# Kernel tuning notes

Measured on AMD Instinct MI355X. Metric: run time of the kernel, lower is better.

## Reference

```python
import jax, jax.numpy as jnp
import numpy as np

B, T, DM, DS = 8, 2048, 1024, 256
BASE_DECAY = 0.05


def _lin(k, out_dim, in_dim):
    return jax.random.normal(k, (out_dim, in_dim), jnp.float32) / np.sqrt(in_dim).astype(np.float32)


def setup_inputs() -> dict:
    key = jax.random.key(0)
    ks = jax.random.split(key, 18)
    return {
        "x": jax.random.normal(ks[0], (B, T, DM), jnp.float32),
        "prev_state": jax.random.normal(ks[1], (B, DS), jnp.float32),
        "W_in": _lin(ks[2], DS, DM),
        "W_x": _lin(ks[3], DS, DM),
        "W_s": _lin(ks[4], DS, DS),
        "W_out": _lin(ks[5], DM, DS),
        "W_gx": _lin(ks[6], DS, DM),
        "b_gx": jax.random.normal(ks[7], (DS,), jnp.float32) * 0.02,
        "W_gs": _lin(ks[8], DS, DS),
        "b_gs": jax.random.normal(ks[9], (DS,), jnp.float32) * 0.02,
        "W_dc": _lin(ks[10], DS, DM + DS),
        "b_dc": jax.random.normal(ks[11], (DS,), jnp.float32) * 0.02,
        "W_pp": _lin(ks[12], DS, 2 * DS),
        "b_pp": jax.random.normal(ks[13], (DS,), jnp.float32) * 0.02,
        "W_pg": _lin(ks[14], DS, DS),
        "b_pg": jax.random.normal(ks[15], (DS,), jnp.float32) * 0.02,
    }


def reference(x, prev_state, W_in, W_x, W_s, W_out, W_gx, b_gx, W_gs, b_gs,
              W_dc, b_dc, W_pp, b_pp, W_pg, b_pg):
    # torch Linear: y = x @ W.T (+ b); W is [out, in]
    lin = lambda v, W: jnp.einsum('bti,oi->bto', v, W)
    Bx, Tx, _ = x.shape
    delta = lin(x, W_in)                                   # [B,T,DS]
    s_prev = jnp.broadcast_to(prev_state[:, None, :], (Bx, Tx, prev_state.shape[-1]))
    ctx = jnp.concatenate([x, s_prev], axis=-1)            # [B,T,DM+DS]
    decay = jnp.exp(-BASE_DECAY * jnp.clip(jax.nn.sigmoid(lin(ctx, W_dc) + b_dc), 0.0, 1.0))
    s_pred = s_prev * decay + delta + lin(x, W_x) + 0.5 * lin(s_prev, W_s)
    perturb_in = jnp.concatenate([s_pred, s_prev], axis=-1)  # [B,T,2*DS]
    perturb_vec = jnp.tanh(lin(perturb_in, W_pp) + b_pp)
    perturb_strength = jax.nn.sigmoid(lin(s_prev, W_pg) + b_pg)
    s_corrected = s_pred + perturb_strength * perturb_vec
    gate_in = jax.nn.sigmoid(lin(x, W_gx) + b_gx)
    gate_state = jax.nn.sigmoid(lin(s_prev, W_gs) + b_gs)
    h = s_corrected * gate_in * gate_state
    out = lin(h, W_out)                                    # [B,T,DM]
    return out, h[:, -1, :]
```

## Files before the change

kernel.cpp:

```cpp
#include <hip/hip_runtime.h>
#include <hip/hip_bf16.h>
#include <math.h>


typedef __attribute__((ext_vector_type(4)))  float f32x4;
typedef __attribute__((ext_vector_type(8)))  short bf16x8;

#define DEV static __device__ __forceinline__

DEV float bf2f(short u) {
  union { float f; unsigned i; } v; v.i = ((unsigned)(unsigned short)u) << 16; return v.f;
}
DEV short f2bf(float f) {
  union { float f; unsigned i; } v; v.f = f;
  unsigned x = v.i;
  return (short)((x + 0x7fffu + ((x >> 16) & 1u)) >> 16);
}
DEV unsigned pk_bf16(float lo, float hi) {
  __hip_bfloat162 h = __float22bfloat162_rn(make_float2(lo, hi));
  return *(unsigned*)&h;
}
DEV float sigmoidf_(float x) { return 1.f / (1.f + expf(-x)); }

DEV void gl16(const short* g, short* l) {
  __builtin_amdgcn_global_load_lds(
      (const __attribute__((address_space(1))) void*)(g),
      (__attribute__((address_space(3))) void*)(l), 16, 0, 0);
}

DEV void stage_tile(const short* gA, const short* gB, short* As, short* Bs,
                    int lda, int ldb, int w, int lane) {
  const int rsub = lane >> 2, kc = (lane & 3) * 8;
#pragma unroll
  for (int j = 0; j < 2; ++j) {
    const int seg = w * 2 + j;
    const int r = seg * 16 + rsub;
    gl16(gA + (size_t)r * lda + kc, As + seg * 512);
    gl16(gB + (size_t)r * ldb + kc, Bs + seg * 512);
  }
}

DEV void kstep(const short* Asb, const short* Bsb, int wr, int wc, int arow, int ag,
               f32x4 (&acc)[4][4]) {
  bf16x8 af[4], bfv[4];
#pragma unroll
  for (int mi = 0; mi < 4; ++mi)
    af[mi] = *(const bf16x8*)(Asb + (wr * 64 + mi * 16 + arow) * 32 + ag * 8);
#pragma unroll
  for (int ni = 0; ni < 4; ++ni)
    bfv[ni] = *(const bf16x8*)(Bsb + (wc * 64 + ni * 16 + arow) * 32 + ag * 8);
#pragma unroll
  for (int mi = 0; mi < 4; ++mi)
#pragma unroll
    for (int ni = 0; ni < 4; ++ni)
      acc[mi][ni] = __builtin_amdgcn_mfma_f32_16x16x32_bf16(af[mi], bfv[ni], acc[mi][ni], 0, 0, 0);
}

static const size_t OFF_Y    = 0;
static const size_t OFF_S    = 25165824;
static const size_t OFF_G    = OFF_S + 8388608;
static const size_t OFF_WCAT = OFF_S + 33554432;
static const size_t OFF_WPP  = OFF_WCAT + 1572864;
static const size_t OFF_WOUT = OFF_WPP + 131072;
static const size_t OFF_VEC  = OFF_WOUT + 524288;

__global__ __launch_bounds__(256, 1) void prep_w_k(const float* __restrict__ W_in,
                                                   const float* __restrict__ W_x,
                                                   const float* __restrict__ W_gx,
                                                   const float* __restrict__ W_dc,
                                                   const float* __restrict__ W_pp,
                                                   const float* __restrict__ W_out,
                                                   short* __restrict__ wcat,
                                                   short* __restrict__ wpp,
                                                   short* __restrict__ wout) {
  const int idx = (int)blockIdx.x * 256 + (int)threadIdx.x;
  const int N_WCAT = 768 * 1024, N_WPP = 256 * 256;
  if (idx < N_WCAT) {
    const int r = idx >> 10, k = idx & 1023;
    float v;
    if (r < 256)      v = W_in[r * 1024 + k] + W_x[r * 1024 + k];
    else if (r < 512) v = W_gx[(r - 256) * 1024 + k];
    else              v = W_dc[(r - 512) * 1280 + k];
    wcat[idx] = f2bf(v);
  } else if (idx < N_WCAT + N_WPP) {
    const int j = idx - N_WCAT, o = j >> 8, k = j & 255;
    wpp[j] = f2bf(W_pp[o * 512 + k]);
  } else {
    const int j = idx - N_WCAT - N_WPP, o = j >> 8, k = j & 255;
    wout[j] = f2bf(W_out[o * 256 + k]);
  }
}

__global__ __launch_bounds__(256, 1) void state_k(const float* __restrict__ prev,
                                                  const float* __restrict__ Ws,
                                                  const float* __restrict__ Wdc,
                                                  const float* __restrict__ bdc,
                                                  const float* __restrict__ Wpp,
                                                  const float* __restrict__ bpp,
                                                  const float* __restrict__ Wpg,
                                                  const float* __restrict__ bpg,
                                                  const float* __restrict__ Wgs,
                                                  const float* __restrict__ bgs,
                                                  float* __restrict__ vecs) {
  const int bid = (int)blockIdx.x;
  const int b = bid / 20, rem = bid % 20, m = rem >> 2, oq = rem & 3;
  const int tid = (int)threadIdx.x, lane = tid & 63, w = tid >> 6;
  const float4 sv = *(const float4*)(prev + b * 256 + lane * 4);
  const float* Wb; const float* bias; int stride, off;
  if (m == 0)      { Wb = Wdc; stride = 1280; off = 1024; bias = bdc; }
  else if (m == 1) { Wb = Ws;  stride = 256;  off = 0;    bias = nullptr; }
  else if (m == 2) { Wb = Wpp; stride = 512;  off = 256;  bias = bpp; }
  else if (m == 3) { Wb = Wpg; stride = 256;  off = 0;    bias = bpg; }
  else             { Wb = Wgs; stride = 256;  off = 0;    bias = bgs; }
  const int o0 = oq * 64 + w * 16;
#pragma unroll 4
  for (int i = 0; i < 16; ++i) {
    const int o = o0 + i;
    const float4 wv = *(const float4*)(Wb + (size_t)o * stride + off + lane * 4);
    float p = wv.x * sv.x + wv.y * sv.y + wv.z * sv.z + wv.w * sv.w;
#pragma unroll
    for (int d = 32; d >= 1; d >>= 1) p += __shfl_xor(p, d, 64);
    if (lane == 0) {
      float r = (m == 1) ? 0.5f * p : p + bias[o];
      if (m >= 3) r = sigmoidf_(r);
      vecs[m * 2048 + b * 256 + o] = r;
    }
  }
}

__global__ __launch_bounds__(256) void gemm1_k(const float* __restrict__ X,
                                               const short* __restrict__ Bm,
                                               short* __restrict__ Y) {
  __shared__ short As[2][4096];
  __shared__ short Bs[2][4096];
  const int tid = (int)threadIdx.x, lane = tid & 63, w = tid >> 6;
  const int wr = w >> 1, wc = w & 1;
  int bid = (int)blockIdx.x;
  bid = (bid & 7) * 96 + (bid >> 3);
  const int m0 = (bid / 6) * 128, n0 = (bid % 6) * 128;
  const short* gB = Bm + (size_t)n0 * 1024;

  const int rsub = lane >> 2, kc = (lane & 3) * 8;
  const float* gX0 = X + (size_t)(m0 + w * 32 + rsub) * 1024 + kc;
  const float* gX1 = X + (size_t)(m0 + w * 32 + 16 + rsub) * 1024 + kc;
  short* lA0 = (short*)As;

  f32x4 acc[4][4];
#pragma unroll
  for (int mi = 0; mi < 4; ++mi)
#pragma unroll
    for (int ni = 0; ni < 4; ++ni)
#pragma unroll
      for (int r = 0; r < 4; ++r) acc[mi][ni][r] = 0.f;

  float4 ra[2][2];
  ra[0][0] = *(const float4*)(gX0);     ra[0][1] = *(const float4*)(gX0 + 4);
  ra[1][0] = *(const float4*)(gX1);     ra[1][1] = *(const float4*)(gX1 + 4);
  {
    const int rB = (w * 2) * 16 + rsub;
    gl16(gB + (size_t)rB * 1024 + kc, Bs[0] + (w * 2) * 512);
    gl16(gB + (size_t)(rB + 16) * 1024 + kc, Bs[0] + (w * 2 + 1) * 512);
  }
#pragma unroll
  for (int j = 0; j < 2; ++j) {
    uint4 pk;
    pk.x = pk_bf16(ra[j][0].x, ra[j][0].y); pk.y = pk_bf16(ra[j][0].z, ra[j][0].w);
    pk.z = pk_bf16(ra[j][1].x, ra[j][1].y); pk.w = pk_bf16(ra[j][1].z, ra[j][1].w);
    *(uint4*)(lA0 + (w * 2 + j) * 512 + lane * 8) = pk;
  }
  __syncthreads();

  const int arow = lane & 15, ag = lane >> 4;
#pragma unroll 1
  for (int t = 0; t < 32; ++t) {
    const int nxt = (t + 1) & 1;
    if (t < 31) {
      ra[0][0] = *(const float4*)(gX0 + (t + 1) * 32);
      ra[0][1] = *(const float4*)(gX0 + (t + 1) * 32 + 4);
      ra[1][0] = *(const float4*)(gX1 + (t + 1) * 32);
      ra[1][1] = *(const float4*)(gX1 + (t + 1) * 32 + 4);
      const int rB = (w * 2) * 16 + rsub;
      gl16(gB + (size_t)rB * 1024 + (t + 1) * 32 + kc, Bs[nxt] + (w * 2) * 512);
      gl16(gB + (size_t)(rB + 16) * 1024 + (t + 1) * 32 + kc, Bs[nxt] + (w * 2 + 1) * 512);
    }
    kstep(As[t & 1], Bs[t & 1], wr, wc, arow, ag, acc);
    if (t < 31) {
#pragma unroll
      for (int j = 0; j < 2; ++j) {
        uint4 pk;
        pk.x = pk_bf16(ra[j][0].x, ra[j][0].y); pk.y = pk_bf16(ra[j][0].z, ra[j][0].w);
        pk.z = pk_bf16(ra[j][1].x, ra[j][1].y); pk.w = pk_bf16(ra[j][1].z, ra[j][1].w);
        *(uint4*)(lA0 + nxt * 4096 + (w * 2 + j) * 512 + lane * 8) = pk;
      }
    }
    __syncthreads();
  }
#pragma unroll
  for (int mi = 0; mi < 4; ++mi)
#pragma unroll
    for (int ni = 0; ni < 4; ++ni) {
      const int col = n0 + wc * 64 + ni * 16 + (lane & 15);
#pragma unroll
      for (int r = 0; r < 4; ++r) {
        const int row = m0 + wr * 64 + mi * 16 + (lane >> 4) * 4 + r;
        Y[(size_t)row * 768 + col] = f2bf(acc[mi][ni][r]);
      }
    }
}

__global__ __launch_bounds__(256, 1) void elem1_k(const short* __restrict__ Y,
                                                  const float* __restrict__ prev,
                                                  const float* __restrict__ bgx,
                                                  const float* __restrict__ vecs,
                                                  short* __restrict__ S,
                                                  short* __restrict__ G) {
  const int t = (int)blockIdx.x * 256 + (int)threadIdx.x;
  const int row = t >> 5, gi = t & 31, j0 = gi * 8;
  const int b = row >> 11;
  const short* yr = Y + (size_t)row * 768;
  const bf16x8 yix = *(const bf16x8*)(yr + j0);
  const bf16x8 ygx = *(const bf16x8*)(yr + 256 + j0);
  const bf16x8 ydc = *(const bf16x8*)(yr + 512 + j0);
  bf16x8 so, go;
#pragma unroll
  for (int j = 0; j < 8; ++j) {
    const int c = b * 256 + j0 + j;
    const float dcl = bf2f(ydc[j]) + vecs[0 * 2048 + c];
    const float dec = expf(-0.05f * sigmoidf_(dcl));
    const float sp = prev[c] * dec + bf2f(yix[j]) + vecs[1 * 2048 + c];
    const float g = sigmoidf_(bf2f(ygx[j]) + bgx[j0 + j]);
    so[j] = f2bf(sp); go[j] = f2bf(g);
  }
  *(bf16x8*)(S + (size_t)row * 256 + j0) = so;
  *(bf16x8*)(G + (size_t)row * 256 + j0) = go;
}

__global__ __launch_bounds__(256) void gemm2h_k(const short* __restrict__ S,
                                                const short* __restrict__ G,
                                                const short* __restrict__ Wpp,
                                                const float* __restrict__ vecs,
                                                short* __restrict__ H,
                                                float* __restrict__ out) {
  __shared__ short As[2][4096];
  __shared__ short Bs[2][4096];
  const int tid = (int)threadIdx.x, lane = tid & 63, w = tid >> 6;
  const int wr = w >> 1, wc = w & 1;
  int bid = (int)blockIdx.x;
  bid = (bid & 7) * 32 + (bid >> 3);
  const int m0 = (bid >> 1) * 128, n0 = (bid & 1) * 128;
  const int b = m0 >> 11;
  const short* gA = S + (size_t)m0 * 256;
  const short* gB = Wpp + (size_t)n0 * 256;

  f32x4 acc[4][4];
#pragma unroll
  for (int mi = 0; mi < 4; ++mi)
#pragma unroll
    for (int ni = 0; ni < 4; ++ni)
#pragma unroll
      for (int r = 0; r < 4; ++r) acc[mi][ni][r] = 0.f;

  stage_tile(gA, gB, As[0], Bs[0], 256, 256, w, lane);
  __syncthreads();
  const int arow = lane & 15, ag = lane >> 4;
#pragma unroll 1
  for (int t = 0; t < 8; ++t) {
    if (t < 7)
      stage_tile(gA + (t + 1) * 32, gB + (t + 1) * 32,
                 As[(t + 1) & 1], Bs[(t + 1) & 1], 256, 256, w, lane);
    kstep(As[t & 1], Bs[t & 1], wr, wc, arow, ag, acc);
    __syncthreads();
  }
#pragma unroll
  for (int mi = 0; mi < 4; ++mi)
#pragma unroll
    for (int ni = 0; ni < 4; ++ni) {
      const int col = n0 + wc * 64 + ni * 16 + (lane & 15);
      const float spp  = vecs[2 * 2048 + b * 256 + col];
      const float pstr = vecs[3 * 2048 + b * 256 + col];
      const float gst  = vecs[4 * 2048 + b * 256 + col];
#pragma unroll
      for (int r = 0; r < 4; ++r) {
        const int row = m0 + wr * 64 + mi * 16 + (lane >> 4) * 4 + r;
        const float pv = tanhf(acc[mi][ni][r] + spp);
        const float sp = bf2f(S[(size_t)row * 256 + col]);
        const float h = (sp + pstr * pv) * bf2f(G[(size_t)row * 256 + col]) * gst;
        H[(size_t)row * 256 + col] = f2bf(h);
        if ((row & 2047) == 2047) out[16777216 + b * 256 + col] = h;
      }
    }
}

__global__ __launch_bounds__(256) void gemm3_k(const short* __restrict__ H,
                                               const short* __restrict__ Wout,
                                               float* __restrict__ out) {
  __shared__ short As[2][4096];
  __shared__ short Bs[2][4096];
  const int tid = (int)threadIdx.x, lane = tid & 63, w = tid >> 6;
  const int wr = w >> 1, wc = w & 1;
  int bid = (int)blockIdx.x;
  bid = (bid & 7) * 128 + (bid >> 3);
  const int m0 = (bid >> 3) * 128, n0 = (bid & 7) * 128;
  const short* gA = H + (size_t)m0 * 256;
  const short* gB = Wout + (size_t)n0 * 256;

  f32x4 acc[4][4];
#pragma unroll
  for (int mi = 0; mi < 4; ++mi)
#pragma unroll
    for (int ni = 0; ni < 4; ++ni)
#pragma unroll
      for (int r = 0; r < 4; ++r) acc[mi][ni][r] = 0.f;

  stage_tile(gA, gB, As[0], Bs[0], 256, 256, w, lane);
  __syncthreads();
  const int arow = lane & 15, ag = lane >> 4;
#pragma unroll 1
  for (int t = 0; t < 8; ++t) {
    if (t < 7)
      stage_tile(gA + (t + 1) * 32, gB + (t + 1) * 32,
                 As[(t + 1) & 1], Bs[(t + 1) & 1], 256, 256, w, lane);
    kstep(As[t & 1], Bs[t & 1], wr, wc, arow, ag, acc);
    __syncthreads();
  }
#pragma unroll
  for (int mi = 0; mi < 4; ++mi)
#pragma unroll
    for (int ni = 0; ni < 4; ++ni) {
      const int col = n0 + wc * 64 + ni * 16 + (lane & 15);
#pragma unroll
      for (int r = 0; r < 4; ++r) {
        const int row = m0 + wr * 64 + mi * 16 + (lane >> 4) * 4 + r;
        out[(size_t)row * 1024 + col] = acc[mi][ni][r];
      }
    }
}

extern "C" void kernel_launch(void* const* d_in, const int* in_sizes, int n_in,
                              void* d_out, int out_size, void* d_ws, size_t ws_size,
                              hipStream_t stream) {
  (void)in_sizes; (void)n_in; (void)out_size; (void)ws_size;
  const float* x      = (const float*)d_in[0];
  const float* prev   = (const float*)d_in[1];
  const float* W_in   = (const float*)d_in[2];
  const float* W_x    = (const float*)d_in[3];
  const float* W_s    = (const float*)d_in[4];
  const float* W_out  = (const float*)d_in[5];
  const float* W_gx   = (const float*)d_in[6];
  const float* b_gx   = (const float*)d_in[7];
  const float* W_gs   = (const float*)d_in[8];
  const float* b_gs   = (const float*)d_in[9];
  const float* W_dc   = (const float*)d_in[10];
  const float* b_dc   = (const float*)d_in[11];
  const float* W_pp   = (const float*)d_in[12];
  const float* b_pp   = (const float*)d_in[13];
  const float* W_pg   = (const float*)d_in[14];
  const float* b_pg   = (const float*)d_in[15];

  char* ws = (char*)d_ws;
  short* Y    = (short*)(ws + OFF_Y);
  short* H    = (short*)(ws + OFF_Y);
  short* S    = (short*)(ws + OFF_S);
  short* G    = (short*)(ws + OFF_G);
  short* wcat = (short*)(ws + OFF_WCAT);
  short* wpp  = (short*)(ws + OFF_WPP);
  short* wout = (short*)(ws + OFF_WOUT);
  float* vecs = (float*)(ws + OFF_VEC);
  float* out  = (float*)d_out;

  prep_w_k<<<4352, 256, 0, stream>>>(W_in, W_x, W_gx, W_dc, W_pp, W_out, wcat, wpp, wout);
  state_k<<<160, 256, 0, stream>>>(prev, W_s, W_dc, b_dc, W_pp, b_pp, W_pg, b_pg, W_gs, b_gs, vecs);
  gemm1_k<<<768, 256, 0, stream>>>(x, wcat, Y);
  elem1_k<<<2048, 256, 0, stream>>>(Y, prev, b_gx, vecs, S, G);
  gemm2h_k<<<256, 256, 0, stream>>>(S, G, wpp, vecs, H, out);
  gemm3_k<<<1024, 256, 0, stream>>>(H, wout, out);
}
```

Measured before the change: 117.7 us.

## Stage fp32 X tiles into LDS via async global_load_lds and convert when reading fragments

The first GEMM used to load fp32 X into registers, pack it to bf16 and write it to LDS by hand. It now copies raw fp32 X tiles straight into LDS with global_load_lds, using an XOR-swizzled column layout to avoid bank conflicts. Conversion to bf16 happens when each MFMA fragment is read from LDS. This removes the register round trip and the LDS store instructions, but doubles LDS footprint and read traffic for A and repeats the conversion on every fragment read.

```diff
diff --git a/kernel.cpp b/kernel.cpp
--- a/kernel.cpp
+++ b/kernel.cpp
@@ -22,7 +22,7 @@
 }
 DEV float sigmoidf_(float x) { return 1.f / (1.f + expf(-x)); }
 
-DEV void gl16(const short* g, short* l) {
+DEV void gl16(const void* g, void* l) {
   __builtin_amdgcn_global_load_lds(
       (const __attribute__((address_space(1))) void*)(g),
       (__attribute__((address_space(3))) void*)(l), 16, 0, 0);
@@ -131,7 +131,7 @@
 __global__ __launch_bounds__(256) void gemm1_k(const float* __restrict__ X,
                                                const short* __restrict__ Bm,
                                                short* __restrict__ Y) {
-  __shared__ short As[2][4096];
+  __shared__ float Af[2][4096];
   __shared__ short Bs[2][4096];
   const int tid = (int)threadIdx.x, lane = tid & 63, w = tid >> 6;
   const int wr = w >> 1, wc = w & 1;
@@ -140,10 +140,16 @@
   const int m0 = (bid / 6) * 128, n0 = (bid % 6) * 128;
   const short* gB = Bm + (size_t)n0 * 1024;
 
+  const int ar = lane >> 3, agr = (lane & 7) ^ ar;
+  const float* gA[4];
+  float* lA[4];
+#pragma unroll
+  for (int j = 0; j < 4; ++j) {
+    const int seg = w * 4 + j;
+    gA[j] = X + (size_t)(m0 + seg * 8 + ar) * 1024 + agr * 4;
+    lA[j] = (float*)Af + seg * 256;
+  }
   const int rsub = lane >> 2, kc = (lane & 3) * 8;
-  const float* gX0 = X + (size_t)(m0 + w * 32 + rsub) * 1024 + kc;
-  const float* gX1 = X + (size_t)(m0 + w * 32 + 16 + rsub) * 1024 + kc;
-  short* lA0 = (short*)As;
 
   f32x4 acc[4][4];
 #pragma unroll
@@ -153,45 +159,50 @@
 #pragma unroll
       for (int r = 0; r < 4; ++r) acc[mi][ni][r] = 0.f;
 
-  float4 ra[2][2];
-  ra[0][0] = *(const float4*)(gX0);     ra[0][1] = *(const float4*)(gX0 + 4);
-  ra[1][0] = *(const float4*)(gX1);     ra[1][1] = *(const float4*)(gX1 + 4);
-  {
-    const int rB = (w * 2) * 16 + rsub;
-    gl16(gB + (size_t)rB * 1024 + kc, Bs[0] + (w * 2) * 512);
-    gl16(gB + (size_t)(rB + 16) * 1024 + kc, Bs[0] + (w * 2 + 1) * 512);
-  }
+#pragma unroll
+  for (int j = 0; j < 4; ++j) gl16(gA[j], lA[j]);
 #pragma unroll
   for (int j = 0; j < 2; ++j) {
-    uint4 pk;
-    pk.x = pk_bf16(ra[j][0].x, ra[j][0].y); pk.y = pk_bf16(ra[j][0].z, ra[j][0].w);
-    pk.z = pk_bf16(ra[j][1].x, ra[j][1].y); pk.w = pk_bf16(ra[j][1].z, ra[j][1].w);
-    *(uint4*)(lA0 + (w * 2 + j) * 512 + lane * 8) = pk;
+    const int rB = (w * 2 + j) * 16 + rsub;
+    gl16(gB + (size_t)rB * 1024 + kc, Bs[0] + (w * 2 + j) * 512);
   }
   __syncthreads();
 
-  const int arow = lane & 15, ag = lane >> 4;
+  const int arow = lane & 15, ag = lane >> 4, r7 = arow & 7;
 #pragma unroll 1
   for (int t = 0; t < 32; ++t) {
-    const int nxt = (t + 1) & 1;
+    const int cur = t & 1, nxt = cur ^ 1;
     if (t < 31) {
-      ra[0][0] = *(const float4*)(gX0 + (t + 1) * 32);
-      ra[0][1] = *(const float4*)(gX0 + (t + 1) * 32 + 4);
-      ra[1][0] = *(const float4*)(gX1 + (t + 1) * 32);
-      ra[1][1] = *(const float4*)(gX1 + (t + 1) * 32 + 4);
-      const int rB = (w * 2) * 16 + rsub;
-      gl16(gB + (size_t)rB * 1024 + (t + 1) * 32 + kc, Bs[nxt] + (w * 2) * 512);
-      gl16(gB + (size_t)(rB + 16) * 1024 + (t + 1) * 32 + kc, Bs[nxt] + (w * 2 + 1) * 512);
-    }
-    kstep(As[t & 1], Bs[t & 1], wr, wc, arow, ag, acc);
-    if (t < 31) {
+#pragma unroll
+      for (int j = 0; j < 4; ++j) gl16(gA[j] + (t + 1) * 32, lA[j] + nxt * 4096);
 #pragma unroll
       for (int j = 0; j < 2; ++j) {
+        const int rB = (w * 2 + j) * 16 + rsub;
+        gl16(gB + (size_t)rB * 1024 + (t + 1) * 32 + kc, Bs[nxt] + (w * 2 + j) * 512);
+      }
+    }
+    {
+      const float* Afb = Af[cur];
+      const short* Bsb = Bs[cur];
+      bf16x8 af[4], bfv[4];
+#pragma unroll
+      for (int mi = 0; mi < 4; ++mi) {
+        const int row = wr * 64 + mi * 16 + arow;
+        const f32x4 lo = *(const f32x4*)(Afb + row * 32 + (((ag * 2)     ^ r7) << 2));
+        const f32x4 hi = *(const f32x4*)(Afb + row * 32 + (((ag * 2 + 1) ^ r7) << 2));
         uint4 pk;
-        pk.x = pk_bf16(ra[j][0].x, ra[j][0].y); pk.y = pk_bf16(ra[j][0].z, ra[j][0].w);
-        pk.z = pk_bf16(ra[j][1].x, ra[j][1].y); pk.w = pk_bf16(ra[j][1].z, ra[j][1].w);
-        *(uint4*)(lA0 + nxt * 4096 + (w * 2 + j) * 512 + lane * 8) = pk;
-      }
+        pk.x = pk_bf16(lo[0], lo[1]); pk.y = pk_bf16(lo[2], lo[3]);
+        pk.z = pk_bf16(hi[0], hi[1]); pk.w = pk_bf16(hi[2], hi[3]);
+        af[mi] = *(bf16x8*)&pk;
+      }
+#pragma unroll
+      for (int ni = 0; ni < 4; ++ni)
+        bfv[ni] = *(const bf16x8*)(Bsb + (wc * 64 + ni * 16 + arow) * 32 + ag * 8);
+#pragma unroll
+      for (int mi = 0; mi < 4; ++mi)
+#pragma unroll
+        for (int ni = 0; ni < 4; ++ni)
+          acc[mi][ni] = __builtin_amdgcn_mfma_f32_16x16x32_bf16(af[mi], bfv[ni], acc[mi][ni], 0, 0, 0);
     }
     __syncthreads();
   }
```

Result: no change. 116.8 us (-0.7%).
